# Optimization experiments

Measured on AMD Instinct MI355X. Metric: run time of the kernel, lower is better.

## Reference

```python
import jax, jax.numpy as jnp
import numpy as np

N_NODES = 50000


def _gcn_conv_mean(x, W, src, dst, deg, dinv_sqrt):
    # GCNConv math: h = x @ W; message = dinv[src]*dinv[dst] * h[src];
    # aggr='mean' -> scatter-sum into dst then divide by in-degree (incl. self loop).
    h = x @ W                                   # [N, outdim]
    norm = dinv_sqrt[src] * dinv_sqrt[dst]      # [E+N]
    msg = norm[:, None] * h[src]                # gather + scale
    agg = jax.ops.segment_sum(msg, dst, num_segments=N_NODES)
    return agg / deg[:, None]                   # mean aggregation (deg >= 1 via self loops)


def setup_inputs() -> dict:
    key = jax.random.key(0)
    k1, k2, k3, k4 = jax.random.split(key, 4)
    x = jax.random.normal(k1, (N_NODES, 64), dtype=jnp.float32)
    edge_index = jax.random.randint(k2, (2, 1600000), 0, N_NODES, dtype=jnp.int64)
    scale = 1.0 / np.sqrt(64.0)
    W1 = jax.random.normal(k3, (64, 64), dtype=jnp.float32) * scale
    W2 = jax.random.normal(k4, (64, 64), dtype=jnp.float32) * scale
    return {"x": x, "edge_index": edge_index, "W1": W1, "W2": W2}


def reference(x, edge_index, W1, W2):
    # add self loops (add_self_loops=True, improved=False -> fill value 1)
    loop = jnp.arange(N_NODES, dtype=edge_index.dtype)
    src = jnp.concatenate([edge_index[0], loop])
    dst = jnp.concatenate([edge_index[1], loop])
    # degree over destination with unit edge weights (gcn_norm)
    deg = jax.ops.segment_sum(jnp.ones_like(src, dtype=x.dtype), dst, num_segments=N_NODES)
    dinv_sqrt = jnp.where(deg > 0, jax.lax.rsqrt(jnp.maximum(deg, 1e-12)), 0.0)
    x1 = jax.nn.relu(_gcn_conv_mean(x, W1, src, dst, deg, dinv_sqrt))
    x2 = jax.nn.sigmoid(_gcn_conv_mean(x, W2, src, dst, deg, dinv_sqrt))
    return x1 * x2
```

## Files before the change

kernel.cpp:

```cpp
#include <hip/hip_runtime.h>

#define NFEAT 64
#define BNODES 64
#define MAXBUCK 1024
#define SORT_LDS 6144
#define KPT 4

__device__ __forceinline__ unsigned short f2bf(float f) {
    unsigned int u = __float_as_uint(f);
    return (unsigned short)((u + 0x7FFFu + ((u >> 16) & 1u)) >> 16);
}
__device__ __forceinline__ float bf2f(unsigned short h) {
    return __uint_as_float(((unsigned int)h) << 16);
}

__global__ void k_zero(int* __restrict__ p, int n) {
    for (int i = threadIdx.x; i < n; i += 1024) p[i] = 0;
}

__global__ __launch_bounds__(256) void k_histb(
        const int* __restrict__ ei, int* __restrict__ bcnt, int E, int nb) {
    __shared__ int h[MAXBUCK];
    __shared__ int s_not64;
    if (threadIdx.x == 0) s_not64 = 0;
    for (int i = threadIdx.x; i < nb; i += 256) h[i] = 0;
    __syncthreads();
    if (ei[2 * threadIdx.x + 1] != 0) s_not64 = 1;
    __syncthreads();
    int is64 = s_not64 ? 0 : 1;
    int per = (E + gridDim.x - 1) / gridDim.x;
    int e0 = blockIdx.x * per;
    int e1 = min(e0 + per, E);
    if (is64) {
        const int2* d64 = (const int2*)ei + E;
        for (int i = e0 + threadIdx.x; i < e1; i += 256)
            atomicAdd(&h[d64[i].x >> 6], 1);
    } else {
        for (int i = e0 + threadIdx.x; i < e1; i += 256)
            atomicAdd(&h[ei[E + i] >> 6], 1);
    }
    __syncthreads();
    for (int i = threadIdx.x; i < nb; i += 256)
        if (h[i]) atomicAdd(&bcnt[i], h[i]);
}

__global__ void k_bscan(const int* __restrict__ bcnt, int* __restrict__ bstart,
                        int* __restrict__ bfill, int nb, int E) {
    __shared__ int s[1024];
    int t = threadIdx.x;
    int mine = (t < nb) ? bcnt[t] : 0;
    s[t] = mine;
    __syncthreads();
    for (int off = 1; off < 1024; off <<= 1) {
        int v = (t >= off) ? s[t - off] : 0;
        __syncthreads();
        s[t] += v;
        __syncthreads();
    }
    if (t < nb) {
        int excl = s[t] - mine;
        bstart[t] = excl;
        bfill[t] = excl;
    }
    if (t == 0) bstart[nb] = E;
}

__global__ __launch_bounds__(1024) void k_part(
        const int* __restrict__ ei, int* __restrict__ bfill,
        unsigned int* __restrict__ edges, int E, int nb) {
    __shared__ int h[MAXBUCK];
    __shared__ int chunk[MAXBUCK];
    __shared__ int cur[MAXBUCK];
    __shared__ int s_not64;
    if (threadIdx.x == 0) s_not64 = 0;
    for (int i = threadIdx.x; i < nb; i += 1024) h[i] = 0;
    __syncthreads();
    if (threadIdx.x < 256 && ei[2 * threadIdx.x + 1] != 0) s_not64 = 1;
    __syncthreads();
    int is64 = s_not64 ? 0 : 1;
    int per = (E + gridDim.x - 1) / gridDim.x;
    int e0 = blockIdx.x * per;
    int e1 = min(e0 + per, E);

    unsigned int ed[KPT];
    if (is64) {
        const int2* s64 = (const int2*)ei;
        const int2* d64 = s64 + E;
#pragma unroll
        for (int k = 0; k < KPT; ++k) {
            int i = e0 + threadIdx.x + k * 1024;
            if (i < e1) {
                unsigned int s = (unsigned int)s64[i].x;
                unsigned int d = (unsigned int)d64[i].x;
                ed[k] = (d << 16) | s;
                atomicAdd(&h[d >> 6], 1);
            }
        }
    } else {
#pragma unroll
        for (int k = 0; k < KPT; ++k) {
            int i = e0 + threadIdx.x + k * 1024;
            if (i < e1) {
                unsigned int s = (unsigned int)ei[i];
                unsigned int d = (unsigned int)ei[E + i];
                ed[k] = (d << 16) | s;
                atomicAdd(&h[d >> 6], 1);
            }
        }
    }
    __syncthreads();
    for (int i = threadIdx.x; i < nb; i += 1024) {
        int c = h[i];
        chunk[i] = c ? atomicAdd(&bfill[i], c) : 0;
        cur[i] = 0;
    }
    __syncthreads();
#pragma unroll
    for (int k = 0; k < KPT; ++k) {
        int i = e0 + threadIdx.x + k * 1024;
        if (i < e1) {
            int b = (int)(ed[k] >> 22);
            int r = atomicAdd(&cur[b], 1);
            edges[chunk[b] + r] = ed[k];
        }
    }
}

template <bool INPLACE>
__global__ __launch_bounds__(256) void k_sort3(
        const unsigned int* __restrict__ edges, const int* __restrict__ bstart,
        const float* __restrict__ x, int* __restrict__ count,
        int* __restrict__ ptr, float* __restrict__ scale,
        unsigned short* __restrict__ y, unsigned short* __restrict__ sorted_src,
        int N, int E) {
    __shared__ int cnt64[BNODES];
    __shared__ int pos64[BNODES];
    __shared__ unsigned int raw[INPLACE ? SORT_LDS : 1];
    int tid = threadIdx.x;
    int vbase = blockIdx.x * BNODES;
    int es = bstart[blockIdx.x];
    int ee = bstart[blockIdx.x + 1];
    int m = ee - es;
    if (tid < BNODES) cnt64[tid] = 0;
    __syncthreads();

    if (INPLACE) {
        int mm = min(m, SORT_LDS);
        for (int i = tid; i < mm; i += 256) {
            unsigned int e = edges[es + i];
            raw[i] = e;
            atomicAdd(&cnt64[(e >> 16) & 63u], 1);
        }
        for (int i = SORT_LDS + tid; i < m; i += 256)
            atomicAdd(&cnt64[(edges[es + i] >> 16) & 63u], 1);
    } else {
        for (int i = tid; i < m; i += 256)
            atomicAdd(&cnt64[(edges[es + i] >> 16) & 63u], 1);
    }
    __syncthreads();

    if (tid < BNODES) {
        int c = cnt64[tid];
        int inc = c;
#pragma unroll
        for (int d = 1; d < 64; d <<= 1) {
            int t2 = __shfl_up(inc, d, 64);
            if (tid >= d) inc += t2;
        }
        int off = inc - c;
        pos64[tid] = es + off;
        int v = vbase + tid;
        if (v < N) {
            count[v] = c;
            ptr[v] = es + off;
            float dg = (float)(c + 1);
            scale[v] = rsqrtf(dg) / dg;
        }
    }
    __syncthreads();

    if (INPLACE) {
        int mm = min(m, SORT_LDS);
        for (int i = tid; i < mm; i += 256) {
            unsigned int e = raw[i];
            int p = atomicAdd(&pos64[(e >> 16) & 63u], 1);
            sorted_src[p] = (unsigned short)(e & 0xFFFFu);
        }
        for (int i = SORT_LDS + tid; i < m; i += 256) {
            unsigned int e = edges[es + i];
            int p = atomicAdd(&pos64[(e >> 16) & 63u], 1);
            sorted_src[p] = (unsigned short)(e & 0xFFFFu);
        }
    } else {
        for (int i = tid; i < m; i += 256) {
            unsigned int e = edges[es + i];
            int p = atomicAdd(&pos64[(e >> 16) & 63u], 1);
            sorted_src[p] = (unsigned short)(e & 0xFFFFu);
        }
    }

    const float4* x4 = (const float4*)x;
    for (int i = tid; i < BNODES * 16; i += 256) {
        int r = i >> 4, j = i & 15;
        int v = vbase + r;
        if (v < N) {
            float dg = (float)(cnt64[r] + 1);
            float dv = rsqrtf(dg);
            float4 q = x4[(size_t)v * 16 + j];
            ushort4 o;
            o.x = f2bf(q.x * dv); o.y = f2bf(q.y * dv);
            o.z = f2bf(q.z * dv); o.w = f2bf(q.w * dv);
            ((ushort4*)y)[(size_t)v * 16 + j] = o;
        }
    }
}

__global__ __launch_bounds__(256) void k_gather3(
        const unsigned int* __restrict__ y32, const float* __restrict__ scale,
        const int* __restrict__ ptr, const int* __restrict__ count,
        const unsigned short* __restrict__ sorted_src,
        float* __restrict__ agg_out, int N) {
    int wave = threadIdx.x >> 6;
    int lane = threadIdx.x & 63;
    int lo = lane & 31;
    int hi = lane >> 5;
    int vbase = blockIdx.x * 16 + wave * 4;

    for (int vi = 0; vi < 4; ++vi) {
        int v = vbase + vi;
        if (v >= N) return;
        int start = ptr[v];
        int cnt = count[v];
        float sc = scale[v];
        float ax0 = 0.f, ay0 = 0.f, ax1 = 0.f, ay1 = 0.f;
        float ax2 = 0.f, ay2 = 0.f, ax3 = 0.f, ay3 = 0.f;
        float ax4 = 0.f, ay4 = 0.f, ax5 = 0.f, ay5 = 0.f;
        float ax6 = 0.f, ay6 = 0.f, ax7 = 0.f, ay7 = 0.f;
        if (hi == 0) {
            unsigned int u = y32[(size_t)v * 32 + lo];
            ax0 += __uint_as_float(u << 16);
            ay0 += __uint_as_float(u & 0xFFFF0000u);
        }

#define ACC(AX, AY, E)                                                 \
        {                                                              \
            unsigned int u_ = y32[(size_t)(E) * 32 + lo];              \
            AX += __uint_as_float(u_ << 16);                           \
            AY += __uint_as_float(u_ & 0xFFFF0000u);                   \
        }

        for (int c = 0; c < cnt; c += 64) {
            int m = min(64, cnt - c);
            int s_l = 0;
            if (lane < m) s_l = (int)sorted_src[start + c + lane];
            int j = 0;
            for (; j + 16 <= m; j += 16) {
                int e0 = __shfl(s_l, j + 0 + hi, 64), e1 = __shfl(s_l, j + 2 + hi, 64);
                int e2 = __shfl(s_l, j + 4 + hi, 64), e3 = __shfl(s_l, j + 6 + hi, 64);
                int e4 = __shfl(s_l, j + 8 + hi, 64), e5 = __shfl(s_l, j + 10 + hi, 64);
                int e6 = __shfl(s_l, j + 12 + hi, 64), e7 = __shfl(s_l, j + 14 + hi, 64);
                ACC(ax0, ay0, e0) ACC(ax1, ay1, e1) ACC(ax2, ay2, e2) ACC(ax3, ay3, e3)
                ACC(ax4, ay4, e4) ACC(ax5, ay5, e5) ACC(ax6, ay6, e6) ACC(ax7, ay7, e7)
            }
            for (; j + 4 <= m; j += 4) {
                int e0 = __shfl(s_l, j + 0 + hi, 64);
                int e1 = __shfl(s_l, j + 2 + hi, 64);
                ACC(ax0, ay0, e0) ACC(ax1, ay1, e1)
            }
            for (; j + 2 <= m; j += 2) {
                int e0 = __shfl(s_l, j + hi, 64);
                ACC(ax0, ay0, e0)
            }
            if (j < m) {
                int e0 = __shfl(s_l, j, 64);
                if (hi == 0) ACC(ax0, ay0, e0)
            }
        }
#undef ACC
        float ax = ((ax0 + ax1) + (ax2 + ax3)) + ((ax4 + ax5) + (ax6 + ax7));
        float ay = ((ay0 + ay1) + (ay2 + ay3)) + ((ay4 + ay5) + (ay6 + ay7));
        ax += __shfl_xor(ax, 32, 64);
        ay += __shfl_xor(ay, 32, 64);
        if (hi == 0) {
            float2 st;
            st.x = ax * sc;
            st.y = ay * sc;
            ((float2*)(agg_out + (size_t)v * NFEAT))[lo] = st;
        }
    }
}

__global__ __launch_bounds__(256) void k_epi6(
        const float* __restrict__ agg, const float* __restrict__ W1,
        const float* __restrict__ W2, float* __restrict__ out, int N) {
    __shared__ float at[64 * 65];
    int tid = threadIdx.x;
    int lane = tid & 63;
    int v0 = blockIdx.x * 64;

    const float4* agg4 = (const float4*)agg;
    for (int i = tid; i < 64 * 16; i += 256) {
        int v = i >> 4, j = i & 15;
        float4 q;
        if (v0 + v < N) q = agg4[(size_t)(v0 + v) * 16 + j];
        else { q.x = q.y = q.z = q.w = 0.f; }
        float* r = &at[v * 65 + j * 4];
        r[0] = q.x; r[1] = q.y; r[2] = q.z; r[3] = q.w;
    }
    __syncthreads();

    int cb = __builtin_amdgcn_readfirstlane((tid >> 6) * 16);
    float acc1[16], acc2[16];
#pragma unroll
    for (int c = 0; c < 16; ++c) { acc1[c] = 0.f; acc2[c] = 0.f; }

    for (int k = 0; k < NFEAT; ++k) {
        float ak = at[lane * 65 + k];
        const float* w1k = W1 + (size_t)k * NFEAT + cb;
        const float* w2k = W2 + (size_t)k * NFEAT + cb;
#pragma unroll
        for (int c = 0; c < 16; ++c) {
            acc1[c] = fmaf(ak, w1k[c], acc1[c]);
            acc2[c] = fmaf(ak, w2k[c], acc2[c]);
        }
    }

    int v = v0 + lane;
    if (v < N) {
        float4* o4 = (float4*)(out + (size_t)v * NFEAT + cb);
#pragma unroll
        for (int g = 0; g < 4; ++g) {
            float4 q;
            float r0 = fmaxf(acc1[4 * g + 0], 0.f), s0 = 1.f / (1.f + __expf(-acc2[4 * g + 0]));
            float r1 = fmaxf(acc1[4 * g + 1], 0.f), s1 = 1.f / (1.f + __expf(-acc2[4 * g + 1]));
            float r2 = fmaxf(acc1[4 * g + 2], 0.f), s2 = 1.f / (1.f + __expf(-acc2[4 * g + 2]));
            float r3 = fmaxf(acc1[4 * g + 3], 0.f), s3 = 1.f / (1.f + __expf(-acc2[4 * g + 3]));
            q.x = r0 * s0; q.y = r1 * s1; q.z = r2 * s2; q.w = r3 * s3;
            o4[g] = q;
        }
    }
}

extern "C" void kernel_launch(void* const* d_in, const int* in_sizes, int n_in,
                              void* d_out, int out_size, void* d_ws, size_t ws_size,
                              hipStream_t stream) {
    const float* x  = (const float*)d_in[0];
    const int*   ei = (const int*)d_in[1];
    const float* W1 = (const float*)d_in[2];
    const float* W2 = (const float*)d_in[3];
    float* out = (float*)d_out;

    const int N = in_sizes[0] / NFEAT;
    const int E = in_sizes[1] / 2;
    const int nb = (N + BNODES - 1) / BNODES;

    char* ws = (char*)d_ws;
    size_t off = 0;
    auto alloc = [&](size_t bytes) {
        char* p = ws + off;
        off = (off + bytes + 255) & ~(size_t)255;
        return p;
    };
    int*   count  = (int*)alloc((size_t)N * 4);
    float* scale  = (float*)alloc((size_t)N * 4);
    int*   ptr    = (int*)alloc((size_t)N * 4);
    int*   bcnt   = (int*)alloc((size_t)MAXBUCK * 4);
    int*   bstart = (int*)alloc((size_t)(MAXBUCK + 1) * 4);
    int*   bfill  = (int*)alloc((size_t)MAXBUCK * 4);

    size_t aggB   = (size_t)N * NFEAT * 4;
    size_t edgeB  = (size_t)E * 4;
    size_t regB   = aggB > edgeB ? aggB : edgeB;
    size_t t1_need = off + regB + (size_t)N * NFEAT * 2 + (size_t)E * 2 + 1024;

    k_zero<<<1, 1024, 0, stream>>>(bcnt, MAXBUCK);
    k_histb<<<256, 256, 0, stream>>>(ei, bcnt, E, nb);
    k_bscan<<<1, 1024, 0, stream>>>(bcnt, bstart, bfill, nb, E);
    int gpart = (E + 1024 * KPT - 1) / (1024 * KPT);
    int gblk = (N + 15) / 16;

    if (ws_size >= t1_need) {
        char* reg = (char*)alloc(regB);
        unsigned int*   edges      = (unsigned int*)reg;
        float*          agg        = (float*)reg;
        unsigned short* y          = (unsigned short*)alloc((size_t)N * NFEAT * 2);
        unsigned short* sorted_src = (unsigned short*)alloc((size_t)E * 2);

        k_part<<<gpart, 1024, 0, stream>>>(ei, bfill, edges, E, nb);
        k_sort3<false><<<nb, 256, 0, stream>>>(edges, bstart, x, count, ptr,
                                               scale, y, sorted_src, N, E);
        k_gather3<<<gblk, 256, 0, stream>>>((const unsigned int*)y, scale, ptr,
                                            count, sorted_src, agg, N);
        k_epi6<<<(N + 63) / 64, 256, 0, stream>>>(agg, W1, W2, out, N);
    } else {
        unsigned int*   edges = (unsigned int*)alloc(edgeB);
        unsigned short* y     = (unsigned short*)alloc((size_t)N * NFEAT * 2);
        unsigned short* sorted_src;
        bool inplace;
        if (ws_size >= off + (size_t)E * 2) {
            sorted_src = (unsigned short*)alloc((size_t)E * 2);
            inplace = false;
        } else {
            sorted_src = (unsigned short*)edges;
            inplace = true;
        }
        k_part<<<gpart, 1024, 0, stream>>>(ei, bfill, edges, E, nb);
        if (inplace) {
            k_sort3<true><<<nb, 256, 0, stream>>>(edges, bstart, x, count, ptr,
                                                  scale, y, sorted_src, N, E);
        } else {
            k_sort3<false><<<nb, 256, 0, stream>>>(edges, bstart, x, count, ptr,
                                                   scale, y, sorted_src, N, E);
        }
        k_gather3<<<gblk, 256, 0, stream>>>((const unsigned int*)y, scale, ptr,
                                            count, sorted_src, out, N);
        k_epi6<<<(N + 63) / 64, 256, 0, stream>>>(out, W1, W2, out, N);
    }
}
```

Before: 104.7 us.

## Fuse neighbor gather with dual-weight epilogue into one kernel via LDS

After: 117.5 us. 12.2% more time.

```diff
diff --git a/kernel.cpp b/kernel.cpp
--- a/kernel.cpp
+++ b/kernel.cpp
@@ -9,9 +9,6 @@
 __device__ __forceinline__ unsigned short f2bf(float f) {
     unsigned int u = __float_as_uint(f);
     return (unsigned short)((u + 0x7FFFu + ((u >> 16) & 1u)) >> 16);
-}
-__device__ __forceinline__ float bf2f(unsigned short h) {
-    return __uint_as_float(((unsigned int)h) << 16);
 }
 
 __global__ void k_zero(int* __restrict__ p, int n) {
@@ -215,101 +212,85 @@
     }
 }
 
-__global__ __launch_bounds__(256) void k_gather3(
+__global__ __launch_bounds__(256) void k_gather_epi(
         const unsigned int* __restrict__ y32, const float* __restrict__ scale,
         const int* __restrict__ ptr, const int* __restrict__ count,
         const unsigned short* __restrict__ sorted_src,
-        float* __restrict__ agg_out, int N) {
-    int wave = threadIdx.x >> 6;
-    int lane = threadIdx.x & 63;
+        const float* __restrict__ W1, const float* __restrict__ W2,
+        float* __restrict__ out, int N) {
+    __shared__ float at[64 * 65];
+    int tid = threadIdx.x;
+    int wave = tid >> 6;
+    int lane = tid & 63;
     int lo = lane & 31;
     int hi = lane >> 5;
-    int vbase = blockIdx.x * 16 + wave * 4;
-
-    for (int vi = 0; vi < 4; ++vi) {
-        int v = vbase + vi;
-        if (v >= N) return;
-        int start = ptr[v];
-        int cnt = count[v];
-        float sc = scale[v];
-        float ax0 = 0.f, ay0 = 0.f, ax1 = 0.f, ay1 = 0.f;
-        float ax2 = 0.f, ay2 = 0.f, ax3 = 0.f, ay3 = 0.f;
-        float ax4 = 0.f, ay4 = 0.f, ax5 = 0.f, ay5 = 0.f;
-        float ax6 = 0.f, ay6 = 0.f, ax7 = 0.f, ay7 = 0.f;
-        if (hi == 0) {
-            unsigned int u = y32[(size_t)v * 32 + lo];
-            ax0 += __uint_as_float(u << 16);
-            ay0 += __uint_as_float(u & 0xFFFF0000u);
-        }
+    int vbase = blockIdx.x * 64;
+
+    for (int vi = 0; vi < 16; ++vi) {
+        int v = vbase + wave * 16 + vi;
+        if (v < N) {
+            int start = ptr[v];
+            int cnt = count[v];
+            float sc = scale[v];
+            float ax0 = 0.f, ay0 = 0.f, ax1 = 0.f, ay1 = 0.f;
+            float ax2 = 0.f, ay2 = 0.f, ax3 = 0.f, ay3 = 0.f;
+            float ax4 = 0.f, ay4 = 0.f, ax5 = 0.f, ay5 = 0.f;
+            float ax6 = 0.f, ay6 = 0.f, ax7 = 0.f, ay7 = 0.f;
+            if (hi == 0) {
+                unsigned int u = y32[(size_t)v * 32 + lo];
+                ax0 += __uint_as_float(u << 16);
+                ay0 += __uint_as_float(u & 0xFFFF0000u);
+            }
 
 #define ACC(AX, AY, E)                                                 \
-        {                                                              \
-            unsigned int u_ = y32[(size_t)(E) * 32 + lo];              \
-            AX += __uint_as_float(u_ << 16);                           \
-            AY += __uint_as_float(u_ & 0xFFFF0000u);                   \
-        }
-
-        for (int c = 0; c < cnt; c += 64) {
-            int m = min(64, cnt - c);
-            int s_l = 0;
-            if (lane < m) s_l = (int)sorted_src[start + c + lane];
-            int j = 0;
-            for (; j + 16 <= m; j += 16) {
-                int e0 = __shfl(s_l, j + 0 + hi, 64), e1 = __shfl(s_l, j + 2 + hi, 64);
-                int e2 = __shfl(s_l, j + 4 + hi, 64), e3 = __shfl(s_l, j + 6 + hi, 64);
-                int e4 = __shfl(s_l, j + 8 + hi, 64), e5 = __shfl(s_l, j + 10 + hi, 64);
-                int e6 = __shfl(s_l, j + 12 + hi, 64), e7 = __shfl(s_l, j + 14 + hi, 64);
-                ACC(ax0, ay0, e0) ACC(ax1, ay1, e1) ACC(ax2, ay2, e2) ACC(ax3, ay3, e3)
-                ACC(ax4, ay4, e4) ACC(ax5, ay5, e5) ACC(ax6, ay6, e6) ACC(ax7, ay7, e7)
-            }
-            for (; j + 4 <= m; j += 4) {
-                int e0 = __shfl(s_l, j + 0 + hi, 64);
-                int e1 = __shfl(s_l, j + 2 + hi, 64);
-                ACC(ax0, ay0, e0) ACC(ax1, ay1, e1)
-            }
-            for (; j + 2 <= m; j += 2) {
-                int e0 = __shfl(s_l, j + hi, 64);
-                ACC(ax0, ay0, e0)
-            }
-            if (j < m) {
-                int e0 = __shfl(s_l, j, 64);
-                if (hi == 0) ACC(ax0, ay0, e0)
-            }
-        }
+            {                                                          \
+                unsigned int u_ = y32[(size_t)(E) * 32 + lo];          \
+                AX += __uint_as_float(u_ << 16);                       \
+                AY += __uint_as_float(u_ & 0xFFFF0000u);               \
+            }
+
+            for (int c = 0; c < cnt; c += 64) {
+                int m = min(64, cnt - c);
+                int s_l = 0;
+                if (lane < m) s_l = (int)sorted_src[start + c + lane];
+                int j = 0;
+                for (; j + 16 <= m; j += 16) {
+                    int e0 = __shfl(s_l, j + 0 + hi, 64), e1 = __shfl(s_l, j + 2 + hi, 64);
+                    int e2 = __shfl(s_l, j + 4 + hi, 64), e3 = __shfl(s_l, j + 6 + hi, 64);
+                    int e4 = __shfl(s_l, j + 8 + hi, 64), e5 = __shfl(s_l, j + 10 + hi, 64);
+                    int e6 = __shfl(s_l, j + 12 + hi, 64), e7 = __shfl(s_l, j + 14 + hi, 64);
+                    ACC(ax0, ay0, e0) ACC(ax1, ay1, e1) ACC(ax2, ay2, e2) ACC(ax3, ay3, e3)
+                    ACC(ax4, ay4, e4) ACC(ax5, ay5, e5) ACC(ax6, ay6, e6) ACC(ax7, ay7, e7)
+                }
+                for (; j + 4 <= m; j += 4) {
+                    int e0 = __shfl(s_l, j + 0 + hi, 64);
+                    int e1 = __shfl(s_l, j + 2 + hi, 64);
+                    ACC(ax0, ay0, e0) ACC(ax1, ay1, e1)
+                }
+                for (; j + 2 <= m; j += 2) {
+                    int e0 = __shfl(s_l, j + hi, 64);
+                    ACC(ax0, ay0, e0)
+                }
+                if (j < m) {
+                    int e0 = __shfl(s_l, j, 64);
+                    if (hi == 0) ACC(ax0, ay0, e0)
+                }
+            }
 #undef ACC
-        float ax = ((ax0 + ax1) + (ax2 + ax3)) + ((ax4 + ax5) + (ax6 + ax7));
-        float ay = ((ay0 + ay1) + (ay2 + ay3)) + ((ay4 + ay5) + (ay6 + ay7));
-        ax += __shfl_xor(ax, 32, 64);
-        ay += __shfl_xor(ay, 32, 64);
-        if (hi == 0) {
-            float2 st;
-            st.x = ax * sc;
-            st.y = ay * sc;
-            ((float2*)(agg_out + (size_t)v * NFEAT))[lo] = st;
-        }
-    }
-}
-
-__global__ __launch_bounds__(256) void k_epi6(
-        const float* __restrict__ agg, const float* __restrict__ W1,
-        const float* __restrict__ W2, float* __restrict__ out, int N) {
-    __shared__ float at[64 * 65];
-    int tid = threadIdx.x;
-    int lane = tid & 63;
-    int v0 = blockIdx.x * 64;
-
-    const float4* agg4 = (const float4*)agg;
-    for (int i = tid; i < 64 * 16; i += 256) {
-        int v = i >> 4, j = i & 15;
-        float4 q;
-        if (v0 + v < N) q = agg4[(size_t)(v0 + v) * 16 + j];
-        else { q.x = q.y = q.z = q.w = 0.f; }
-        float* r = &at[v * 65 + j * 4];
-        r[0] = q.x; r[1] = q.y; r[2] = q.z; r[3] = q.w;
-    }
-    __syncthreads();
-
-    int cb = __builtin_amdgcn_readfirstlane((tid >> 6) * 16);
+            float ax = ((ax0 + ax1) + (ax2 + ax3)) + ((ax4 + ax5) + (ax6 + ax7));
+            float ay = ((ay0 + ay1) + (ay2 + ay3)) + ((ay4 + ay5) + (ay6 + ay7));
+            ax += __shfl_xor(ax, 32, 64);
+            ay += __shfl_xor(ay, 32, 64);
+            if (hi == 0) {
+                int r = wave * 16 + vi;
+                at[r * 65 + 2 * lo + 0] = ax * sc;
+                at[r * 65 + 2 * lo + 1] = ay * sc;
+            }
+        }
+    }
+    __syncthreads();
+
+    int cb = __builtin_amdgcn_readfirstlane(wave * 16);
     float acc1[16], acc2[16];
 #pragma unroll
     for (int c = 0; c < 16; ++c) { acc1[c] = 0.f; acc2[c] = 0.f; }
@@ -325,7 +306,7 @@
         }
     }
 
-    int v = v0 + lane;
+    int v = vbase + lane;
     if (v < N) {
         float4* o4 = (float4*)(out + (size_t)v * NFEAT + cb);
 #pragma unroll
@@ -367,53 +348,31 @@
     int*   bcnt   = (int*)alloc((size_t)MAXBUCK * 4);
     int*   bstart = (int*)alloc((size_t)(MAXBUCK + 1) * 4);
     int*   bfill  = (int*)alloc((size_t)MAXBUCK * 4);
-
-    size_t aggB   = (size_t)N * NFEAT * 4;
-    size_t edgeB  = (size_t)E * 4;
-    size_t regB   = aggB > edgeB ? aggB : edgeB;
-    size_t t1_need = off + regB + (size_t)N * NFEAT * 2 + (size_t)E * 2 + 1024;
+    unsigned int*   edges = (unsigned int*)alloc((size_t)E * 4);
+    unsigned short* y     = (unsigned short*)alloc((size_t)N * NFEAT * 2);
+
+    unsigned short* sorted_src;
+    bool inplace;
+    if (ws_size >= off + (size_t)E * 2) {
+        sorted_src = (unsigned short*)alloc((size_t)E * 2);
+        inplace = false;
+    } else {
+        sorted_src = (unsigned short*)edges;
+        inplace = true;
+    }
 
     k_zero<<<1, 1024, 0, stream>>>(bcnt, MAXBUCK);
     k_histb<<<256, 256, 0, stream>>>(ei, bcnt, E, nb);
     k_bscan<<<1, 1024, 0, stream>>>(bcnt, bstart, bfill, nb, E);
     int gpart = (E + 1024 * KPT - 1) / (1024 * KPT);
-    int gblk = (N + 15) / 16;
-
-    if (ws_size >= t1_need) {
-        char* reg = (char*)alloc(regB);
-        unsigned int*   edges      = (unsigned int*)reg;
-        float*          agg        = (float*)reg;
-        unsigned short* y          = (unsigned short*)alloc((size_t)N * NFEAT * 2);
-        unsigned short* sorted_src = (unsigned short*)alloc((size_t)E * 2);
-
-        k_part<<<gpart, 1024, 0, stream>>>(ei, bfill, edges, E, nb);
+    k_part<<<gpart, 1024, 0, stream>>>(ei, bfill, edges, E, nb);
+    if (inplace) {
+        k_sort3<true><<<nb, 256, 0, stream>>>(edges, bstart, x, count, ptr,
+                                              scale, y, sorted_src, N, E);
+    } else {
         k_sort3<false><<<nb, 256, 0, stream>>>(edges, bstart, x, count, ptr,
                                                scale, y, sorted_src, N, E);
-        k_gather3<<<gblk, 256, 0, stream>>>((const unsigned int*)y, scale, ptr,
-                                            count, sorted_src, agg, N);
-        k_epi6<<<(N + 63) / 64, 256, 0, stream>>>(agg, W1, W2, out, N);
-    } else {
-        unsigned int*   edges = (unsigned int*)alloc(edgeB);
-        unsigned short* y     = (unsigned short*)alloc((size_t)N * NFEAT * 2);
-        unsigned short* sorted_src;
-        bool inplace;
-        if (ws_size >= off + (size_t)E * 2) {
-            sorted_src = (unsigned short*)alloc((size_t)E * 2);
-            inplace = false;
-        } else {
-            sorted_src = (unsigned short*)edges;
-            inplace = true;
-        }
-        k_part<<<gpart, 1024, 0, stream>>>(ei, bfill, edges, E, nb);
-        if (inplace) {
-            k_sort3<true><<<nb, 256, 0, stream>>>(edges, bstart, x, count, ptr,
-                                                  scale, y, sorted_src, N, E);
-        } else {
-            k_sort3<false><<<nb, 256, 0, stream>>>(edges, bstart, x, count, ptr,
-                                                   scale, y, sorted_src, N, E);
-        }
-        k_gather3<<<gblk, 256, 0, stream>>>((const unsigned int*)y, scale, ptr,
-                                            count, sorted_src, out, N);
-        k_epi6<<<(N + 63) / 64, 256, 0, stream>>>(out, W1, W2, out, N);
-    }
-}
+    }
+    k_gather_epi<<<(N + 63) / 64, 256, 0, stream>>>(
+        (const unsigned int*)y, scale, ptr, count, sorted_src, W1, W2, out, N);
+}
```
